# Kernel tuning notes

Hardware: AMD Instinct MI355X
Metric: run time of the kernel (lower is better)

## Reference

```python
import jax, jax.numpy as jnp
import numpy as np

D_MODEL = 1024
N_HEADS = 16
HEAD_DIM = D_MODEL // N_HEADS
ROPE_BASE = 10000.0


def _rope_cos_sin(seq_len, head_dim, dtype):
    inv_freq = 1.0 / (ROPE_BASE ** (jnp.arange(0, head_dim, 2, dtype=jnp.float32) / head_dim))
    t = jnp.arange(seq_len, dtype=jnp.float32)
    freqs = jnp.outer(t, inv_freq)            # [S, head_dim//2]
    emb = jnp.concatenate([freqs, freqs], axis=-1)  # [S, head_dim]
    return jnp.cos(emb).astype(dtype), jnp.sin(emb).astype(dtype)


def _rotate_half(x):
    half = x.shape[-1] // 2
    return jnp.concatenate([-x[..., half:], x[..., :half]], axis=-1)


def setup_inputs() -> dict:
    key = jax.random.key(0)
    k0, k1, k2, k3, k4 = jax.random.split(key, 5)
    B, S = 2, 2048
    scale = 1.0 / np.sqrt(D_MODEL)
    return {
        "hidden_states": jax.random.normal(k0, (B, S, D_MODEL), dtype=jnp.float32),
        "w_q": jax.random.normal(k1, (D_MODEL, D_MODEL), dtype=jnp.float32) * scale,
        "w_k": jax.random.normal(k2, (D_MODEL, D_MODEL), dtype=jnp.float32) * scale,
        "w_v": jax.random.normal(k3, (D_MODEL, D_MODEL), dtype=jnp.float32) * scale,
        "w_o": jax.random.normal(k4, (D_MODEL, D_MODEL), dtype=jnp.float32) * scale,
    }


def reference(hidden_states, w_q, w_k, w_v, w_o):
    B, S, D = hidden_states.shape
    H, hd = N_HEADS, HEAD_DIM

    def proj(w):
        # nn.Linear: x @ w.T -> [B, H, S, hd]
        return (hidden_states @ w.T).reshape(B, S, H, hd).transpose(0, 2, 1, 3)

    q, k, v = proj(w_q), proj(w_k), proj(w_v)

    cos, sin = _rope_cos_sin(S, hd, hidden_states.dtype)
    cos = cos[None, None]  # [1,1,S,hd]
    sin = sin[None, None]
    q = q * cos + _rotate_half(q) * sin
    k = k * cos + _rotate_half(k) * sin

    scores = jnp.einsum("bhqd,bhkd->bhqk", q, k) / jnp.sqrt(jnp.asarray(hd, hidden_states.dtype))
    attn = jax.nn.softmax(scores, axis=-1)
    out = jnp.einsum("bhqk,bhkd->bhqd", attn, v)
    out = out.transpose(0, 2, 1, 3).reshape(B, S, D)
    return out @ w_o.T
```

## Files before the change

kernel.cpp:

```cpp
#include <hip/hip_runtime.h>
#include <math.h>

#define SEQ 2048
#define NTOK 4096
#define DM 1024

typedef __bf16 bf16x8 __attribute__((ext_vector_type(8)));
typedef __bf16 bf16x4 __attribute__((ext_vector_type(4)));
typedef float  f32x4  __attribute__((ext_vector_type(4)));

__device__ __forceinline__ void gll16(const void* g, void* l) {
    __builtin_amdgcn_global_load_lds(
        (const __attribute__((address_space(1))) void*)g,
        (__attribute__((address_space(3))) void*)l, 16, 0, 0);
}

__device__ __forceinline__ f32x4 mfma16(bf16x8 a, bf16x8 b, f32x4 c) {
    return __builtin_amdgcn_mfma_f32_16x16x32_bf16(a, b, c, 0, 0, 0);
}

__global__ void conv_all(const float* __restrict__ hs, const float* __restrict__ wq,
                         const float* __restrict__ wk, const float* __restrict__ wv,
                         const float* __restrict__ wo, __bf16* hsb, __bf16* wqb,
                         __bf16* wkb, __bf16* wvb, __bf16* wob,
                         float* __restrict__ ct, float* __restrict__ st) {
    if (blockIdx.x >= 8192) {
        int t = (blockIdx.x - 8192) * 256 + threadIdx.x;
        int s = t >> 6, d = t & 63;
        int e = d & 31;
        float invf = 1.0f / powf(10000.0f, (float)e / 32.0f);
        float ang  = (float)s * invf;
        double a   = (double)ang;
        ct[s * 64 + d] = (float)cos(a);
        st[s * 64 + d] = (float)sin(a);
        return;
    }
    long i = (long)blockIdx.x * 256 + threadIdx.x;
    const long H4 = (long)NTOK * DM / 4;
    const float* src; __bf16* dst; long off;
    float scale = 1.0f;
    if (i < H4) { src = hs; dst = hsb; off = i; }
    else {
        long t = i - H4;
        int wsel = (int)(t >> 18);
        off = t & ((1L << 18) - 1);
        switch (wsel) {
            case 0:  src = wq; dst = wqb; scale = 0.125f; break;
            case 1:  src = wk; dst = wkb; break;
            case 2:  src = wv; dst = wvb; break;
            default: src = wo; dst = wob; break;
        }
    }
    float4 v = ((const float4*)src)[off];
    __bf16* o = dst + off * 4;
    o[0] = (__bf16)(v.x * scale); o[1] = (__bf16)(v.y * scale);
    o[2] = (__bf16)(v.z * scale); o[3] = (__bf16)(v.w * scale);
}

template <typename OutT, bool ROPE>
__device__ __forceinline__ void gemm_core(__bf16* __restrict__ L,
                                          const __bf16* __restrict__ A,
                                          const __bf16* __restrict__ B,
                                          OutT* __restrict__ C, int N,
                                          const float* __restrict__ ct,
                                          const float* __restrict__ st,
                                          long bm, long bn) {
    const int tid  = threadIdx.x;
    const int lane = tid & 63;
    const int wid  = tid >> 6;
    const int l15  = lane & 15, lg = lane >> 4;
    const int wr = (wid >> 1) * 64, wc = (wid & 1) * 64;

    f32x4 acc[4][4];
    #pragma unroll
    for (int i = 0; i < 4; ++i)
        #pragma unroll
        for (int j = 0; j < 4; ++j) acc[i][j] = 0;

    const int i0 = tid, i1 = tid + 256;
    const __bf16* Ag0 = A + (bm + (i0 >> 2)) * 1024 + (((i0 & 3) ^ ((i0 >> 3) & 3)) * 8);
    const __bf16* Ag1 = A + (bm + (i1 >> 2)) * 1024 + (((i1 & 3) ^ ((i1 >> 3) & 3)) * 8);
    const __bf16* Bg0 = B + (bn + (i0 >> 2)) * 1024 + (((i0 & 3) ^ ((i0 >> 3) & 3)) * 8);
    const __bf16* Bg1 = B + (bn + (i1 >> 2)) * 1024 + (((i1 & 3) ^ ((i1 >> 3) & 3)) * 8);

    auto stage = [&](int buf, int k0) {
        gll16(Ag0 + k0, &L[buf * 8192 + tid * 8]);
        gll16(Ag1 + k0, &L[buf * 8192 + 2048 + tid * 8]);
        gll16(Bg0 + k0, &L[buf * 8192 + 4096 + tid * 8]);
        gll16(Bg1 + k0, &L[buf * 8192 + 6144 + tid * 8]);
    };

    const int rbase = l15 * 32 + ((lg ^ ((l15 >> 1) & 3)) * 8);

    auto compute = [&](int buf) {
        const int AS = buf * 8192, BS = buf * 8192 + 4096;
        bf16x8 a[4], b[4];
        #pragma unroll
        for (int i = 0; i < 4; ++i)
            a[i] = *(const bf16x8*)(L + AS + (wr + i * 16) * 32 + rbase);
        #pragma unroll
        for (int j = 0; j < 4; ++j)
            b[j] = *(const bf16x8*)(L + BS + (wc + j * 16) * 32 + rbase);
        __builtin_amdgcn_s_setprio(1);
        #pragma unroll
        for (int i = 0; i < 4; ++i)
            #pragma unroll
            for (int j = 0; j < 4; ++j)
                acc[i][j] = mfma16(a[i], b[j], acc[i][j]);
        __builtin_amdgcn_s_setprio(0);
    };

    stage(0, 0);
    stage(1, 32);

    #pragma unroll 1
    for (int tt = 0; tt < 30; tt += 3) {
        asm volatile("s_waitcnt vmcnt(4)" ::: "memory");
        __builtin_amdgcn_s_barrier();
        __builtin_amdgcn_sched_barrier(0);
        stage(2, (tt + 2) * 32); compute(0);

        asm volatile("s_waitcnt vmcnt(4)" ::: "memory");
        __builtin_amdgcn_s_barrier();
        __builtin_amdgcn_sched_barrier(0);
        stage(0, (tt + 3) * 32); compute(1);

        asm volatile("s_waitcnt vmcnt(4)" ::: "memory");
        __builtin_amdgcn_s_barrier();
        __builtin_amdgcn_sched_barrier(0);
        stage(1, (tt + 4) * 32); compute(2);
    }
    asm volatile("s_waitcnt vmcnt(4)" ::: "memory");
    __builtin_amdgcn_s_barrier();
    __builtin_amdgcn_sched_barrier(0);
    compute(0);
    asm volatile("s_waitcnt vmcnt(0)" ::: "memory");
    __builtin_amdgcn_s_barrier();
    __builtin_amdgcn_sched_barrier(0);
    compute(1);

    if constexpr (ROPE) {
        #pragma unroll
        for (int i = 0; i < 4; ++i)
            #pragma unroll
            for (int j = 0; j < 2; ++j)
                #pragma unroll
                for (int r = 0; r < 4; ++r) {
                    long row = bm + wr + i * 16 + lg * 4 + r;
                    int  s   = (int)(row & (SEQ - 1));
                    int  d   = j * 16 + l15;
                    float c  = ct[s * 64 + d];
                    float sn = st[s * 64 + d];
                    float x0 = acc[i][j][r], x1 = acc[i][j + 2][r];
                    long col = bn + wc + j * 16 + l15;
                    C[row * N + col]      = (OutT)(x0 * c - x1 * sn);
                    C[row * N + col + 32] = (OutT)(x1 * c + x0 * sn);
                }
    } else {
        #pragma unroll
        for (int i = 0; i < 4; ++i)
            #pragma unroll
            for (int j = 0; j < 4; ++j)
                #pragma unroll
                for (int r = 0; r < 4; ++r) {
                    long row = bm + wr + i * 16 + lg * 4 + r;
                    long col = bn + wc + j * 16 + l15;
                    C[row * N + col] = (OutT)acc[i][j][r];
                }
    }
}

__global__ __launch_bounds__(256) void gemm_qkv(const __bf16* __restrict__ hsb,
                                                const __bf16* __restrict__ wqb,
                                                const __bf16* __restrict__ wkb,
                                                const __bf16* __restrict__ wvb,
                                                __bf16* __restrict__ Qb,
                                                __bf16* __restrict__ Kb,
                                                __bf16* __restrict__ Vtb,
                                                const float* __restrict__ ct,
                                                const float* __restrict__ st) {
    __shared__ __bf16 L[24576];
    const int bid = blockIdx.x;
    const int w = (bid & 7) * 96 + (bid >> 3);
    const int z = w >> 8, rem = w & 255;
    if (z < 2)
        gemm_core<__bf16, true>(L, hsb, z ? wkb : wqb, z ? Kb : Qb, 1024, ct, st,
                                (long)(rem >> 3) * 128, (long)(rem & 7) * 128);
    else
        gemm_core<__bf16, false>(L, wvb, hsb, Vtb, 4096, nullptr, nullptr,
                                 (long)(rem & 7) * 128, (long)(rem >> 3) * 128);
}

__global__ __launch_bounds__(256) void gemm_out(const __bf16* __restrict__ A,
                                                const __bf16* __restrict__ B,
                                                float* __restrict__ C) {
    __shared__ __bf16 L[24576];
    const int bid = blockIdx.x;
    const int w = (bid & 7) * 32 + (bid >> 3);
    gemm_core<float, false>(L, A, B, C, 1024, nullptr, nullptr,
                            (long)(w >> 3) * 128, (long)(w & 7) * 128);
}

#define FIXED_M 16.0f

__global__ __launch_bounds__(512) void flash9(const __bf16* __restrict__ Qb,
                                              const __bf16* __restrict__ Kb,
                                              const __bf16* __restrict__ Vt,
                                              __bf16* __restrict__ Ob) {
    __shared__ __bf16 L[24576];
    const int h = blockIdx.x, b = blockIdx.y, qt = blockIdx.z;
    const int tid = threadIdx.x, lane = tid & 63, w = tid >> 6;
    const int wq = w >> 1, wk = w & 1;
    const int l15 = lane & 15, lg = lane >> 4;

    const int x7  = l15 & 7;
    const int kb0 = wk * 2048 + l15 * 64 + ((lg ^ x7) * 8);
    const int kb1 = wk * 2048 + l15 * 64 + (((4 + lg) ^ x7) * 8);
    const int vb0 = l15 * 64 + (((wk * 4 + lg) ^ x7) * 8);
    const int prb = 16384 + (wq * 32 + l15) * 64 + (((wk * 4 + lg) ^ x7) * 8);
    int wb[2];
    #pragma unroll
    for (int j = 0; j < 2; ++j)
        wb[j] = 16384 + (wq * 32 + l15) * 64 +
                (((wk * 4 + j * 2 + (lg >> 1)) ^ x7) * 8) + (lg & 1) * 4;

    bf16x8 qf[2][2];
    #pragma unroll
    for (int qa = 0; qa < 2; ++qa) {
        long qrow = (long)b * SEQ + qt * 128 + wq * 32 + qa * 16 + l15;
        qf[qa][0] = *(const bf16x8*)(Qb + qrow * DM + h * 64 + lg * 8);
        qf[qa][1] = *(const bf16x8*)(Qb + qrow * DM + h * 64 + 32 + lg * 8);
    }

    f32x4 oacc[2][4];
    #pragma unroll
    for (int qa = 0; qa < 2; ++qa)
        #pragma unroll
        for (int i = 0; i < 4; ++i) oacc[qa][i] = 0;
    f32x4 lvec[2] = {0, 0};

    const int srow = tid >> 3;
    const int sgz  = (tid & 7) ^ (srow & 7);
    const __bf16* kp = Kb + ((long)b * SEQ + srow) * DM + h * 64 + sgz * 8;
    const __bf16* vp = Vt + ((long)h * 64 + srow) * NTOK + (long)b * SEQ + sgz * 8;

    auto stage = [&](int bf) {
        gll16(kp, &L[bf * 4096 + tid * 8]);
        gll16(vp, &L[8192 + bf * 4096 + tid * 8]);
        kp += (long)64 * DM;
        vp += 64;
    };

    const float L2E = 1.4426950408889634f;
    const float mL  = FIXED_M * L2E;

    auto compute = [&](int bf) {
        const int KS = bf * 4096, VS = 8192 + bf * 4096;
        f32x4 sc[2][2];
        __builtin_amdgcn_s_setprio(1);
        #pragma unroll
        for (int j = 0; j < 2; ++j) {
            bf16x8 ka0 = *(const bf16x8*)(L + KS + j * 1024 + kb0);
            bf16x8 ka1 = *(const bf16x8*)(L + KS + j * 1024 + kb1);
            #pragma unroll
            for (int qa = 0; qa < 2; ++qa) {
                f32x4 z = 0;
                z = mfma16(ka0, qf[qa][0], z);
                z = mfma16(ka1, qf[qa][1], z);
                sc[qa][j] = z;
            }
        }
        __builtin_amdgcn_s_setprio(0);

        #pragma unroll
        for (int qa = 0; qa < 2; ++qa) {
            f32x4 rv = 0;
            #pragma unroll
            for (int j = 0; j < 2; ++j) {
                #pragma unroll
                for (int r = 0; r < 4; ++r)
                    sc[qa][j][r] = __builtin_amdgcn_exp2f(
                        __builtin_fmaf(sc[qa][j][r], L2E, -mL));
                rv += sc[qa][j];
            }
            lvec[qa] += rv;
            #pragma unroll
            for (int j = 0; j < 2; ++j) {
                bf16x4 p4;
                p4[0] = (__bf16)sc[qa][j][0]; p4[1] = (__bf16)sc[qa][j][1];
                p4[2] = (__bf16)sc[qa][j][2]; p4[3] = (__bf16)sc[qa][j][3];
                *(bf16x4*)(L + wb[j] + qa * 1024) = p4;
            }
        }

        bf16x8 pb[2];
        #pragma unroll
        for (int qa = 0; qa < 2; ++qa)
            pb[qa] = *(const bf16x8*)(L + prb + qa * 1024);
        __builtin_amdgcn_s_setprio(1);
        #pragma unroll
        for (int i = 0; i < 4; ++i) {
            bf16x8 vb = *(const bf16x8*)(L + VS + i * 1024 + vb0);
            #pragma unroll
            for (int qa = 0; qa < 2; ++qa)
                oacc[qa][i] = mfma16(vb, pb[qa], oacc[qa][i]);
        }
        __builtin_amdgcn_s_setprio(0);
    };

    stage(0);
    __syncthreads();

    #pragma unroll 1
    for (int t = 0; t < 32; t += 2) {
        stage(1);
        compute(0);
        __syncthreads();
        if (t + 2 < 32) stage(0);
        compute(1);
        __syncthreads();
    }

    float lh[2];
    #pragma unroll
    for (int qa = 0; qa < 2; ++qa) {
        float l = (lvec[qa][0] + lvec[qa][1]) + (lvec[qa][2] + lvec[qa][3]);
        l += __shfl_xor(l, 16);
        l += __shfl_xor(l, 32);
        lh[qa] = l;
    }

    float* df = (float*)L;
    float* lf = df + 9216;
    if (wk) {
        const int base = (wq * 64 + lane) * 36;
        #pragma unroll
        for (int qa = 0; qa < 2; ++qa) {
            #pragma unroll
            for (int i = 0; i < 4; ++i)
                *(f32x4*)(df + base + qa * 16 + i * 4) = oacc[qa][i];
            if (lg == 0) lf[wq * 32 + qa * 16 + l15] = lh[qa];
        }
    }
    __syncthreads();
    if (!wk) {
        const int base = (wq * 64 + lane) * 36;
        #pragma unroll
        for (int qa = 0; qa < 2; ++qa) {
            float lt = lh[qa] + lf[wq * 32 + qa * 16 + l15];
            float linv = 1.0f / lt;
            const long tok = (long)b * SEQ + qt * 128 + wq * 32 + qa * 16 + l15;
            #pragma unroll
            for (int i = 0; i < 4; ++i) {
                f32x4 ot = oacc[qa][i] + *(const f32x4*)(df + base + qa * 16 + i * 4);
                bf16x4 o4;
                #pragma unroll
                for (int r = 0; r < 4; ++r) o4[r] = (__bf16)(ot[r] * linv);
                *(bf16x4*)(Ob + tok * DM + h * 64 + i * 16 + lg * 4) = o4;
            }
        }
    }
}

extern "C" void kernel_launch(void* const* d_in, const int* in_sizes, int n_in,
                              void* d_out, int out_size, void* d_ws, size_t ws_size,
                              hipStream_t stream) {
    const float* hs = (const float*)d_in[0];
    const float* wq = (const float*)d_in[1];
    const float* wk = (const float*)d_in[2];
    const float* wv = (const float*)d_in[3];
    const float* wo = (const float*)d_in[4];
    float* out = (float*)d_out;

    __bf16* hsb = (__bf16*)d_ws;
    __bf16* wqb = hsb + (long)NTOK * DM;
    __bf16* wkb = wqb + DM * DM;
    __bf16* wvb = wkb + DM * DM;
    __bf16* wob = wvb + DM * DM;
    __bf16* Qb  = wob + DM * DM;
    __bf16* Kb  = Qb + (long)NTOK * DM;
    __bf16* Vtb = Kb + (long)NTOK * DM;
    float*  ct  = (float*)(Vtb + (long)NTOK * DM);
    float*  st  = ct + SEQ * 64;

    conv_all<<<dim3(8704), 256, 0, stream>>>(hs, wq, wk, wv, wo,
                                             hsb, wqb, wkb, wvb, wob, ct, st);

    gemm_qkv<<<dim3(768), 256, 0, stream>>>(hsb, wqb, wkb, wvb,
                                            Qb, Kb, Vtb, ct, st);

    flash9<<<dim3(16, 2, SEQ / 128), 512, 0, stream>>>(Qb, Kb, Vtb, Qb);

    gemm_out<<<dim3(256), 256, 0, stream>>>(Qb, wob, out);
}
```

Baseline: 106.3 us.

## Load K/V tiles directly into registers instead of LDS double-buffering

```diff
diff --git a/kernel.cpp b/kernel.cpp
--- a/kernel.cpp
+++ b/kernel.cpp
@@ -203,25 +203,22 @@
 
 #define FIXED_M 16.0f
 
-__global__ __launch_bounds__(512) void flash9(const __bf16* __restrict__ Qb,
-                                              const __bf16* __restrict__ Kb,
-                                              const __bf16* __restrict__ Vt,
-                                              __bf16* __restrict__ Ob) {
-    __shared__ __bf16 L[24576];
+__global__ __launch_bounds__(512) void flash13(const __bf16* __restrict__ Qb,
+                                               const __bf16* __restrict__ Kb,
+                                               const __bf16* __restrict__ Vt,
+                                               __bf16* __restrict__ Ob) {
+    __shared__ __bf16 L[18688];
     const int h = blockIdx.x, b = blockIdx.y, qt = blockIdx.z;
     const int tid = threadIdx.x, lane = tid & 63, w = tid >> 6;
     const int wq = w >> 1, wk = w & 1;
     const int l15 = lane & 15, lg = lane >> 4;
-
     const int x7  = l15 & 7;
-    const int kb0 = wk * 2048 + l15 * 64 + ((lg ^ x7) * 8);
-    const int kb1 = wk * 2048 + l15 * 64 + (((4 + lg) ^ x7) * 8);
-    const int vb0 = l15 * 64 + (((wk * 4 + lg) ^ x7) * 8);
-    const int prb = 16384 + (wq * 32 + l15) * 64 + (((wk * 4 + lg) ^ x7) * 8);
+
+    const int prb = (wq * 32 + l15) * 64 + (((wk * 4 + lg) ^ x7) * 8);
     int wb[2];
     #pragma unroll
     for (int j = 0; j < 2; ++j)
-        wb[j] = 16384 + (wq * 32 + l15) * 64 +
+        wb[j] = (wq * 32 + l15) * 64 +
                 (((wk * 4 + j * 2 + (lg >> 1)) ^ x7) * 8) + (lg & 1) * 4;
 
     bf16x8 qf[2][2];
@@ -239,37 +236,38 @@
         for (int i = 0; i < 4; ++i) oacc[qa][i] = 0;
     f32x4 lvec[2] = {0, 0};
 
-    const int srow = tid >> 3;
-    const int sgz  = (tid & 7) ^ (srow & 7);
-    const __bf16* kp = Kb + ((long)b * SEQ + srow) * DM + h * 64 + sgz * 8;
-    const __bf16* vp = Vt + ((long)h * 64 + srow) * NTOK + (long)b * SEQ + sgz * 8;
-
-    auto stage = [&](int bf) {
-        gll16(kp, &L[bf * 4096 + tid * 8]);
-        gll16(vp, &L[8192 + bf * 4096 + tid * 8]);
-        kp += (long)64 * DM;
-        vp += 64;
-    };
+    const __bf16* kg = Kb + ((long)b * SEQ + wk * 32 + l15) * DM + h * 64 + lg * 8;
+    const __bf16* vg = Vt + ((long)h * 64 + l15) * NTOK + (long)b * SEQ
+                          + wk * 32 + lg * 8;
 
     const float L2E = 1.4426950408889634f;
     const float mL  = FIXED_M * L2E;
 
-    auto compute = [&](int bf) {
-        const int KS = bf * 4096, VS = 8192 + bf * 4096;
+    #pragma unroll 1
+    for (int t = 0; t < 32; ++t) {
+        bf16x8 ka[2][2], va[4];
+        #pragma unroll
+        for (int j = 0; j < 2; ++j) {
+            ka[j][0] = *(const bf16x8*)(kg + (long)(j * 16) * DM);
+            ka[j][1] = *(const bf16x8*)(kg + (long)(j * 16) * DM + 32);
+        }
+        #pragma unroll
+        for (int i = 0; i < 4; ++i)
+            va[i] = *(const bf16x8*)(vg + (long)(i * 16) * NTOK);
+        kg += (long)64 * DM;
+        vg += 64;
+
         f32x4 sc[2][2];
         __builtin_amdgcn_s_setprio(1);
         #pragma unroll
-        for (int j = 0; j < 2; ++j) {
-            bf16x8 ka0 = *(const bf16x8*)(L + KS + j * 1024 + kb0);
-            bf16x8 ka1 = *(const bf16x8*)(L + KS + j * 1024 + kb1);
+        for (int j = 0; j < 2; ++j)
             #pragma unroll
             for (int qa = 0; qa < 2; ++qa) {
                 f32x4 z = 0;
-                z = mfma16(ka0, qf[qa][0], z);
-                z = mfma16(ka1, qf[qa][1], z);
+                z = mfma16(ka[j][0], qf[qa][0], z);
+                z = mfma16(ka[j][1], qf[qa][1], z);
                 sc[qa][j] = z;
             }
-        }
         __builtin_amdgcn_s_setprio(0);
 
         #pragma unroll
@@ -299,26 +297,11 @@
             pb[qa] = *(const bf16x8*)(L + prb + qa * 1024);
         __builtin_amdgcn_s_setprio(1);
         #pragma unroll
-        for (int i = 0; i < 4; ++i) {
-            bf16x8 vb = *(const bf16x8*)(L + VS + i * 1024 + vb0);
+        for (int i = 0; i < 4; ++i)
             #pragma unroll
             for (int qa = 0; qa < 2; ++qa)
-                oacc[qa][i] = mfma16(vb, pb[qa], oacc[qa][i]);
-        }
+                oacc[qa][i] = mfma16(va[i], pb[qa], oacc[qa][i]);
         __builtin_amdgcn_s_setprio(0);
-    };
-
-    stage(0);
-    __syncthreads();
-
-    #pragma unroll 1
-    for (int t = 0; t < 32; t += 2) {
-        stage(1);
-        compute(0);
-        __syncthreads();
-        if (t + 2 < 32) stage(0);
-        compute(1);
-        __syncthreads();
     }
 
     float lh[2];
@@ -330,6 +313,7 @@
         lh[qa] = l;
     }
 
+    __syncthreads();
     float* df = (float*)L;
     float* lf = df + 9216;
     if (wk) {
@@ -389,7 +373,7 @@
     gemm_qkv<<<dim3(768), 256, 0, stream>>>(hsb, wqb, wkb, wvb,
                                             Qb, Kb, Vtb, ct, st);
 
-    flash9<<<dim3(16, 2, SEQ / 128), 512, 0, stream>>>(Qb, Kb, Vtb, Qb);
+    flash13<<<dim3(16, 2, SEQ / 128), 512, 0, stream>>>(Qb, Kb, Vtb, Qb);
 
     gemm_out<<<dim3(256), 256, 0, stream>>>(Qb, wob, out);
 }
```

Result: slower. 178.3 us (+67.8%).
